# Performance work log

Hardware: AMD Instinct MI355X
Metric: run time of the kernel (lower is better)

## Reference

```python
import jax, jax.numpy as jnp
import numpy as np

NUM_FILLERS = 50257
NUM_ROLES = 512
FILLER_DIM = 256  # D1
ROLE_DIM = 256    # D2
OUT_DIM = 1024
B, S = 64, 128


def setup_inputs() -> dict:
    key = jax.random.key(0)
    k1, k2, k3, k4, k5, k6 = jax.random.split(key, 6)
    fillers = jax.random.randint(k1, (B, S), 0, NUM_FILLERS)
    roles = jax.random.randint(k2, (B, S), 0, NUM_ROLES)
    filler_table = jax.random.normal(k3, (NUM_FILLERS, FILLER_DIM), dtype=jnp.float32)
    role_table = jax.random.normal(k4, (NUM_ROLES, ROLE_DIM), dtype=jnp.float32)
    # nn.Linear(filler_dim*role_dim, final_layer_width)
    lim = 1.0 / np.sqrt(FILLER_DIM * ROLE_DIM)
    W = jax.random.uniform(k5, (OUT_DIM, FILLER_DIM * ROLE_DIM), minval=-lim, maxval=lim, dtype=jnp.float32)
    b = jax.random.uniform(k6, (OUT_DIM,), minval=-lim, maxval=lim, dtype=jnp.float32)
    return {"fillers": fillers, "roles": roles, "filler_table": filler_table,
            "role_table": role_table, "W": W, "b": b}


def reference(fillers, roles, filler_table, role_table, W, b):
    # Embedding lookups: [B, S, D1] and [B, S, D2]
    f = filler_table[fillers]
    r = role_table[roles]
    # Sum over S of flattened outer products f_s (x) r_s -> [B, D1, D2]
    # (equivalent to the original's S*B rank-1 bmm + sum over S, fused as one GEMM)
    tp = jnp.einsum('bsd,bse->bde', f, r)
    tp = tp.reshape(f.shape[0], FILLER_DIM * ROLE_DIM)  # [B, D1*D2]
    # Final linear layer
    return tp @ W.T + b
```

## Files before the change

### kernel.cpp

```cpp
#include <hip/hip_runtime.h>
#include <hip/hip_bf16.h>

#define B_DIM 64
#define S_DIM 128
#define D1    256
#define D2    256
#define KTOT  65536
#define NOUT  1024

#define KSPLIT 128
#define KCHUNK (KTOT / KSPLIT)
#define KITERS (KCHUNK / 32)

typedef __attribute__((ext_vector_type(8))) short bf16x8;
typedef __attribute__((ext_vector_type(4))) float f32x4;

__device__ inline unsigned pack2bf16(float lo, float hi) {
    unsigned ulo = __float_as_uint(lo);
    unsigned uhi = __float_as_uint(hi);
    ulo = (ulo + 0x8000u) >> 16;
    uhi = (uhi + 0x8000u) & 0xffff0000u;
    return ulo | uhi;
}

__global__ __launch_bounds__(256) void tp_kernel(const int* __restrict__ fillers,
                                                 const int* __restrict__ roles,
                                                 const float* __restrict__ ftab,
                                                 const float* __restrict__ rtab,
                                                 unsigned short* __restrict__ tp) {
    const int b     = blockIdx.x;
    const int dbase = blockIdx.y * 32;
    __shared__ float f_sh[S_DIM][32];
    __shared__ int   ridx[S_DIM];
    const int t = threadIdx.x;

    const int* fb = fillers + b * S_DIM;
    for (int i = t; i < S_DIM * 32; i += 256) {
        int s = i >> 5, dl = i & 31;
        f_sh[s][dl] = ftab[(long)fb[s] * D1 + dbase + dl];
    }
    if (t < S_DIM) ridx[t] = roles[b * S_DIM + t];
    __syncthreads();

    const int dsub = t >> 6;
    const int et   = t & 63;
    float acc[8][4];
#pragma unroll
    for (int i = 0; i < 8; ++i)
#pragma unroll
        for (int j = 0; j < 4; ++j) acc[i][j] = 0.f;

    for (int s = 0; s < S_DIM; ++s) {
        const float4 rv = *(const float4*)(rtab + ridx[s] * D2 + et * 4);
        const float4 f0 = *(const float4*)&f_sh[s][dsub * 8];
        const float4 f1 = *(const float4*)&f_sh[s][dsub * 8 + 4];
        float fv[8] = {f0.x, f0.y, f0.z, f0.w, f1.x, f1.y, f1.z, f1.w};
        float rr[4] = {rv.x, rv.y, rv.z, rv.w};
#pragma unroll
        for (int dl = 0; dl < 8; ++dl)
#pragma unroll
            for (int c = 0; c < 4; ++c) acc[dl][c] += fv[dl] * rr[c];
    }

    unsigned short* dst = tp + (size_t)b * KTOT + (size_t)(dbase + dsub * 8) * D2 + et * 4;
#pragma unroll
    for (int dl = 0; dl < 8; ++dl) {
        uint2 pp;
        pp.x = pack2bf16(acc[dl][0], acc[dl][1]);
        pp.y = pack2bf16(acc[dl][2], acc[dl][3]);
        *(uint2*)(dst + (size_t)dl * D2) = pp;
    }
}

__global__ __launch_bounds__(256) void gemm_kernel(const unsigned short* __restrict__ tp,
                                                   const float* __restrict__ W,
                                                   float* __restrict__ part) {
    const int nt  = blockIdx.x;
    const int ks  = blockIdx.y;
    const int w   = threadIdx.x >> 6;
    const int L   = threadIdx.x & 63;
    const int l16 = L & 15;
    const int lq  = L >> 4;
    const int ncol = nt * 64 + w * 16;
    const int k0   = ks * KCHUNK + lq * 8;

    const unsigned short* tpp = tp + (size_t)l16 * KTOT + k0;
    const float*          wp  = W + (size_t)(ncol + l16) * KTOT + k0;

    f32x4 acc[4];
#pragma unroll
    for (int mt = 0; mt < 4; ++mt) acc[mt] = (f32x4){0.f, 0.f, 0.f, 0.f};

    bf16x8 ca0 = *(const bf16x8*)(tpp);
    bf16x8 ca1 = *(const bf16x8*)(tpp + 16 * KTOT);
    bf16x8 ca2 = *(const bf16x8*)(tpp + 32 * KTOT);
    bf16x8 ca3 = *(const bf16x8*)(tpp + 48 * KTOT);
    float4 cw0 = *(const float4*)(wp);
    float4 cw1 = *(const float4*)(wp + 4);

#pragma unroll
    for (int kk = 0; kk < KITERS; ++kk) {
        bf16x8 na0, na1, na2, na3;
        float4 nw0, nw1;
        if (kk + 1 < KITERS) {
            const unsigned short* tn = tpp + (kk + 1) * 32;
            const float*          wn = wp + (kk + 1) * 32;
            na0 = *(const bf16x8*)(tn);
            na1 = *(const bf16x8*)(tn + 16 * KTOT);
            na2 = *(const bf16x8*)(tn + 32 * KTOT);
            na3 = *(const bf16x8*)(tn + 48 * KTOT);
            nw0 = *(const float4*)(wn);
            nw1 = *(const float4*)(wn + 4);
        }
        int4 pb;
        pb.x = (int)pack2bf16(cw0.x, cw0.y);
        pb.y = (int)pack2bf16(cw0.z, cw0.w);
        pb.z = (int)pack2bf16(cw1.x, cw1.y);
        pb.w = (int)pack2bf16(cw1.z, cw1.w);
        bf16x8 bw = *(bf16x8*)&pb;
        acc[0] = __builtin_amdgcn_mfma_f32_16x16x32_bf16(ca0, bw, acc[0], 0, 0, 0);
        acc[1] = __builtin_amdgcn_mfma_f32_16x16x32_bf16(ca1, bw, acc[1], 0, 0, 0);
        acc[2] = __builtin_amdgcn_mfma_f32_16x16x32_bf16(ca2, bw, acc[2], 0, 0, 0);
        acc[3] = __builtin_amdgcn_mfma_f32_16x16x32_bf16(ca3, bw, acc[3], 0, 0, 0);
        ca0 = na0; ca1 = na1; ca2 = na2; ca3 = na3;
        cw0 = nw0; cw1 = nw1;
    }

    float* pp = part + (size_t)ks * (B_DIM * NOUT) + ncol + l16;
#pragma unroll
    for (int mt = 0; mt < 4; ++mt)
#pragma unroll
        for (int r = 0; r < 4; ++r)
            pp[(size_t)(mt * 16 + lq * 4 + r) * NOUT] = acc[mt][r];
}

__global__ __launch_bounds__(256) void reduce_kernel(const float* __restrict__ part,
                                                     const float* __restrict__ bias,
                                                     float* __restrict__ out) {
    const int i    = blockIdx.x * 256 + threadIdx.x;
    const size_t o = (size_t)i * 4;
    const float* p = part + o;
    f32x4 a0 = {0.f, 0.f, 0.f, 0.f};
    f32x4 a1 = {0.f, 0.f, 0.f, 0.f};
#pragma unroll 8
    for (int ks = 0; ks < KSPLIT; ks += 2) {
        f32x4 x = *(const f32x4*)(p + (size_t)ks * (B_DIM * NOUT));
        f32x4 y = *(const f32x4*)(p + (size_t)(ks + 1) * (B_DIM * NOUT));
        a0 += x;
        a1 += y;
    }
    f32x4 bv = *(const f32x4*)(bias + (o & (NOUT - 1)));
    f32x4 r  = a0 + a1 + bv;
    *(f32x4*)(out + o) = r;
}

extern "C" void kernel_launch(void* const* d_in, const int* in_sizes, int n_in,
                              void* d_out, int out_size, void* d_ws, size_t ws_size,
                              hipStream_t stream) {
    const int*   fillers = (const int*)d_in[0];
    const int*   roles   = (const int*)d_in[1];
    const float* ftab    = (const float*)d_in[2];
    const float* rtab    = (const float*)d_in[3];
    const float* W       = (const float*)d_in[4];
    const float* bias    = (const float*)d_in[5];
    float* out = (float*)d_out;

    float*          part = (float*)d_ws;
    unsigned short* tp   = (unsigned short*)((char*)d_ws + (size_t)KSPLIT * B_DIM * NOUT * 4);

    hipLaunchKernelGGL(tp_kernel, dim3(B_DIM, 8), dim3(256), 0, stream,
                       fillers, roles, ftab, rtab, tp);
    hipLaunchKernelGGL(gemm_kernel, dim3(16, KSPLIT), dim3(256), 0, stream, tp, W, part);
    hipLaunchKernelGGL(reduce_kernel, dim3(64), dim3(256), 0, stream, part, bias, out);
}
```

Before: 453.2 us.

## Stage W tiles through LDS with coalesced loads and halve K split

```diff
diff --git a/kernel.cpp b/kernel.cpp
--- a/kernel.cpp
+++ b/kernel.cpp
@@ -8,9 +8,12 @@
 #define KTOT  65536
 #define NOUT  1024
 
-#define KSPLIT 128
+#define KSPLIT 64
 #define KCHUNK (KTOT / KSPLIT)
-#define KITERS (KCHUNK / 32)
+#define BK     128
+#define BKITERS (KCHUNK / BK)
+#define KSTEPS  (BK / 32)
+#define WPAD   16
 
 typedef __attribute__((ext_vector_type(8))) short bf16x8;
 typedef __attribute__((ext_vector_type(4))) float f32x4;
@@ -72,58 +75,67 @@
     }
 }
 
-__global__ __launch_bounds__(256) void gemm_kernel(const unsigned short* __restrict__ tp,
-                                                   const float* __restrict__ W,
-                                                   float* __restrict__ part) {
+__global__ __launch_bounds__(256, 4) void gemm_kernel(const unsigned short* __restrict__ tp,
+                                                      const float* __restrict__ W,
+                                                      float* __restrict__ part) {
     const int nt  = blockIdx.x;
     const int ks  = blockIdx.y;
     const int w   = threadIdx.x >> 6;
     const int L   = threadIdx.x & 63;
     const int l16 = L & 15;
     const int lq  = L >> 4;
-    const int ncol = nt * 64 + w * 16;
-    const int k0   = ks * KCHUNK + lq * 8;
+    const int t   = threadIdx.x;
+    const int ncol  = nt * 64 + w * 16;
+    const int kbase = ks * KCHUNK;
 
-    const unsigned short* tpp = tp + (size_t)l16 * KTOT + k0;
-    const float*          wp  = W + (size_t)(ncol + l16) * KTOT + k0;
+    __shared__ unsigned short wlds[64][BK + WPAD];
+
+    const int srow = t >> 5;
+    const int sc4  = t & 31;
+    const float* wsrc = W + (size_t)(nt * 64 + srow) * KTOT + kbase + sc4 * 4;
+
+    const unsigned short* tpp = tp + (size_t)l16 * KTOT + kbase + lq * 8;
 
     f32x4 acc[4];
 #pragma unroll
     for (int mt = 0; mt < 4; ++mt) acc[mt] = (f32x4){0.f, 0.f, 0.f, 0.f};
 
-    bf16x8 ca0 = *(const bf16x8*)(tpp);
-    bf16x8 ca1 = *(const bf16x8*)(tpp + 16 * KTOT);
-    bf16x8 ca2 = *(const bf16x8*)(tpp + 32 * KTOT);
-    bf16x8 ca3 = *(const bf16x8*)(tpp + 48 * KTOT);
-    float4 cw0 = *(const float4*)(wp);
-    float4 cw1 = *(const float4*)(wp + 4);
+    float4 wreg[8];
+#pragma unroll
+    for (int i = 0; i < 8; ++i)
+        wreg[i] = *(const float4*)(wsrc + (size_t)(8 * i) * KTOT);
+
+    for (int bk = 0; bk < BKITERS; ++bk) {
+#pragma unroll
+        for (int i = 0; i < 8; ++i) {
+            uint2 pp;
+            pp.x = pack2bf16(wreg[i].x, wreg[i].y);
+            pp.y = pack2bf16(wreg[i].z, wreg[i].w);
+            *(uint2*)&wlds[srow + 8 * i][sc4 * 4] = pp;
+        }
+        __syncthreads();
+
+        if (bk + 1 < BKITERS) {
+            const float* wn = wsrc + (bk + 1) * BK;
+#pragma unroll
+            for (int i = 0; i < 8; ++i)
+                wreg[i] = *(const float4*)(wn + (size_t)(8 * i) * KTOT);
+        }
 
 #pragma unroll
-    for (int kk = 0; kk < KITERS; ++kk) {
-        bf16x8 na0, na1, na2, na3;
-        float4 nw0, nw1;
-        if (kk + 1 < KITERS) {
-            const unsigned short* tn = tpp + (kk + 1) * 32;
-            const float*          wn = wp + (kk + 1) * 32;
-            na0 = *(const bf16x8*)(tn);
-            na1 = *(const bf16x8*)(tn + 16 * KTOT);
-            na2 = *(const bf16x8*)(tn + 32 * KTOT);
-            na3 = *(const bf16x8*)(tn + 48 * KTOT);
-            nw0 = *(const float4*)(wn);
-            nw1 = *(const float4*)(wn + 4);
+        for (int kk = 0; kk < KSTEPS; ++kk) {
+            const int koff = bk * BK + kk * 32;
+            bf16x8 a0 = *(const bf16x8*)(tpp + koff);
+            bf16x8 a1 = *(const bf16x8*)(tpp + koff + 16 * KTOT);
+            bf16x8 a2 = *(const bf16x8*)(tpp + koff + 32 * KTOT);
+            bf16x8 a3 = *(const bf16x8*)(tpp + koff + 48 * KTOT);
+            bf16x8 bw = *(const bf16x8*)&wlds[w * 16 + l16][kk * 32 + lq * 8];
+            acc[0] = __builtin_amdgcn_mfma_f32_16x16x32_bf16(a0, bw, acc[0], 0, 0, 0);
+            acc[1] = __builtin_amdgcn_mfma_f32_16x16x32_bf16(a1, bw, acc[1], 0, 0, 0);
+            acc[2] = __builtin_amdgcn_mfma_f32_16x16x32_bf16(a2, bw, acc[2], 0, 0, 0);
+            acc[3] = __builtin_amdgcn_mfma_f32_16x16x32_bf16(a3, bw, acc[3], 0, 0, 0);
         }
-        int4 pb;
-        pb.x = (int)pack2bf16(cw0.x, cw0.y);
-        pb.y = (int)pack2bf16(cw0.z, cw0.w);
-        pb.z = (int)pack2bf16(cw1.x, cw1.y);
-        pb.w = (int)pack2bf16(cw1.z, cw1.w);
-        bf16x8 bw = *(bf16x8*)&pb;
-        acc[0] = __builtin_amdgcn_mfma_f32_16x16x32_bf16(ca0, bw, acc[0], 0, 0, 0);
-        acc[1] = __builtin_amdgcn_mfma_f32_16x16x32_bf16(ca1, bw, acc[1], 0, 0, 0);
-        acc[2] = __builtin_amdgcn_mfma_f32_16x16x32_bf16(ca2, bw, acc[2], 0, 0, 0);
-        acc[3] = __builtin_amdgcn_mfma_f32_16x16x32_bf16(ca3, bw, acc[3], 0, 0, 0);
-        ca0 = na0; ca1 = na1; ca2 = na2; ca3 = na3;
-        cw0 = nw0; cw1 = nw1;
+        __syncthreads();
     }
 
     float* pp = part + (size_t)ks * (B_DIM * NOUT) + ncol + l16;
```

After: 445.6 us. Within noise of the previous version (-1.7%).
